# Kernel tuning notes

Measured on AMD Instinct MI355X. Metric: run time of the kernel, lower is better.

Reference implementation:

```python
import jax, jax.numpy as jnp
import numpy as np

N_NODES = 100000


def sage_conv(x, src, dst, w_self, w_nei, b):
    # mean aggregation over incoming edges (src -> dst)
    agg = jax.ops.segment_sum(x[src], dst, num_segments=N_NODES)          # [N, d]
    deg = jax.ops.segment_sum(jnp.ones((src.shape[0], 1), x.dtype), dst,
                              num_segments=N_NODES)                        # [N, 1]
    mean = agg / jnp.maximum(deg, 1.0)
    return x @ w_self + mean @ w_nei + b


def setup_inputs() -> dict:
    key = jax.random.key(0)
    ks = jax.random.split(key, 12)
    d_in, d_hid, d_out = 64, 64, 64
    E = 1600000
    s = lambda d: 1.0 / np.sqrt(d)
    return {
        "x": jax.random.normal(ks[0], (N_NODES, d_in), jnp.float32),
        "edge_index": jax.random.randint(ks[1], (2, E), 0, N_NODES, jnp.int64),
        "w_self1": jax.random.normal(ks[2], (d_in, d_hid), jnp.float32) * s(d_in),
        "w_nei1": jax.random.normal(ks[3], (d_in, d_hid), jnp.float32) * s(d_in),
        "b1": jnp.zeros((d_hid,), jnp.float32),
        "w_self2": jax.random.normal(ks[4], (d_hid, d_hid), jnp.float32) * s(d_hid),
        "w_nei2": jax.random.normal(ks[5], (d_hid, d_hid), jnp.float32) * s(d_hid),
        "b2": jnp.zeros((d_hid,), jnp.float32),
        "w_self3": jax.random.normal(ks[6], (d_hid, d_out), jnp.float32) * s(d_hid),
        "w_nei3": jax.random.normal(ks[7], (d_hid, d_out), jnp.float32) * s(d_hid),
        "b3": jnp.zeros((d_out,), jnp.float32),
    }


def reference(x, edge_index, w_self1, w_nei1, b1, w_self2, w_nei2, b2,
              w_self3, w_nei3, b3):
    src, dst = edge_index[0], edge_index[1]
    h = jax.nn.relu(sage_conv(x, src, dst, w_self1, w_nei1, b1))
    h = jax.nn.relu(sage_conv(h, src, dst, w_self2, w_nei2, b2))
    h = sage_conv(h, src, dst, w_self3, w_nei3, b3)
    return h
```

## Files before the change

### kernel.cpp

```cpp
#include <hip/hip_runtime.h>
#include <hip/hip_bf16.h>

#define PB   512
#define BN   64
#define CAP  1344

typedef short bf16x8 __attribute__((ext_vector_type(8)));
typedef float f32x4  __attribute__((ext_vector_type(4)));

__device__ __forceinline__ unsigned short f2bf(float f) {
    unsigned u = __float_as_uint(f);
    u += 0x7FFFu + ((u >> 16) & 1u);
    return (unsigned short)(u >> 16);
}

__global__ __launch_bounds__(256) void build_and_prep(
        const int* __restrict__ src, const int* __restrict__ dst,
        int* __restrict__ gcount, int* __restrict__ pairs, int E, int NB,
        const float* __restrict__ x, unsigned short* __restrict__ xb, int n8,
        const float* __restrict__ Ws1, const float* __restrict__ Wn1,
        const float* __restrict__ Ws2, const float* __restrict__ Wn2,
        const float* __restrict__ Ws3, const float* __restrict__ Wn3,
        unsigned short* __restrict__ bw) {
    const int tid = threadIdx.x;
    if (blockIdx.x < PB) {
        __shared__ int h[1664];
        for (int i = tid; i < NB; i += 256) h[i] = 0;
        __syncthreads();
        const int per = (E + PB - 1) / PB;
        const int s = blockIdx.x * per;
        const int e = min(E, s + per);
        for (int i = s + tid; i < e; i += 256) atomicAdd(&h[dst[i] >> 6], 1);
        __syncthreads();
        for (int b = tid; b < NB; b += 256) {
            const int c = h[b];
            h[b] = (c > 0) ? atomicAdd(&gcount[b], c) : 0;
        }
        __syncthreads();
        for (int i = s + tid; i < e; i += 256) {
            const int d = dst[i];
            const int b = d >> 6;
            const int slot = atomicAdd(&h[b], 1);
            if (slot < CAP)
                pairs[(size_t)b * CAP + slot] = src[i] | ((d & 63) << 20);
        }
    } else if (blockIdx.x < PB + 96) {
        const int i = (blockIdx.x - PB) * 256 + tid;
        const int w = i >> 13;
        const int r = i & 8191;
        const float* Ws = (w == 0) ? Ws1 : (w == 1) ? Ws2 : Ws3;
        const float* Wn = (w == 0) ? Wn1 : (w == 1) ? Wn2 : Wn3;
        const int j = r & 7;
        const int L = (r >> 3) & 63;
        const int t = (r >> 9) & 3;
        const int s = r >> 11;
        const int k = s * 32 + ((L >> 4) << 3) + j;
        const int n = t * 16 + (L & 15);
        const float v = (k < 64) ? Ws[k * 64 + n] : Wn[(k - 64) * 64 + n];
        bw[i] = f2bf(v);
    } else {
        const int g = (blockIdx.x - PB - 96) * 256 + tid;
        if (g >= n8) return;
        const float4 v0 = *(const float4*)(x + (size_t)g * 8);
        const float4 v1 = *(const float4*)(x + (size_t)g * 8 + 4);
        uint4 o;
        o.x = (unsigned)f2bf(v0.x) | ((unsigned)f2bf(v0.y) << 16);
        o.y = (unsigned)f2bf(v0.z) | ((unsigned)f2bf(v0.w) << 16);
        o.z = (unsigned)f2bf(v1.x) | ((unsigned)f2bf(v1.y) << 16);
        o.w = (unsigned)f2bf(v1.z) | ((unsigned)f2bf(v1.w) << 16);
        *(uint4*)(xb + (size_t)g * 8) = o;
    }
}

__global__ __launch_bounds__(256) void csr_finalize(const int* __restrict__ pairs,
                                                    const int* __restrict__ gcount,
                                                    int2* __restrict__ rowrange,
                                                    int* __restrict__ col, int N) {
    __shared__ int sp[CAP];
    __shared__ int h[64];
    __shared__ int tmp[64];
    __shared__ int cur[64];
    const int tid = threadIdx.x;
    const int b = blockIdx.x;
    const size_t base = (size_t)b * CAP;
    const int cnt = min(gcount[b], (int)CAP);

    for (int i = tid; i < cnt; i += 256) sp[i] = pairs[base + i];
    if (tid < 64) h[tid] = 0;
    __syncthreads();
    for (int i = tid; i < cnt; i += 256)
        atomicAdd(&h[(sp[i] >> 20) & 63], 1);
    __syncthreads();
    if (tid < 64) tmp[tid] = h[tid];
    __syncthreads();
    for (int off = 1; off < 64; off <<= 1) {
        int t = (tid >= off && tid < 64) ? tmp[tid - off] : 0;
        __syncthreads();
        if (tid < 64) tmp[tid] += t;
        __syncthreads();
    }
    if (tid < 64) {
        const int v = h[tid];
        const int excl = tmp[tid] - v;
        const int node = (b << 6) + tid;
        if (node < N) rowrange[node] = make_int2((int)base + excl, (int)base + excl + v);
        cur[tid] = excl;
    }
    __syncthreads();
    for (int i = tid; i < cnt; i += 256) {
        const int p = sp[i];
        const int slot = atomicAdd(&cur[(p >> 20) & 63], 1);
        col[base + slot] = p & 0xFFFFF;
    }
}

#define ACC8U(A, V)                                                   \
    A[0] += __uint_as_float((V).x << 16);                             \
    A[1] += __uint_as_float((V).x & 0xFFFF0000u);                     \
    A[2] += __uint_as_float((V).y << 16);                             \
    A[3] += __uint_as_float((V).y & 0xFFFF0000u);                     \
    A[4] += __uint_as_float((V).z << 16);                             \
    A[5] += __uint_as_float((V).z & 0xFFFF0000u);                     \
    A[6] += __uint_as_float((V).w << 16);                             \
    A[7] += __uint_as_float((V).w & 0xFFFF0000u);

__global__ __launch_bounds__(128) void sage_fused_kernel(
        const unsigned short* __restrict__ xin, const int* __restrict__ col,
        const int2* __restrict__ rowrange,
        const unsigned short* __restrict__ bswp, const float* __restrict__ bias,
        unsigned short* __restrict__ outb,
        float* __restrict__ outf,
        int N, int do_relu) {
    __shared__ __align__(16) unsigned short smean[32][72];

    const int tid = threadIdx.x;
    const int node0 = blockIdx.x * 32;
    const int lane = tid & 63;

    {
        const int nl = tid >> 2;
        const int node = node0 + nl;
        const int o = (tid & 3) * 8;
        float accA[8] = {0.f}, accB[8] = {0.f};
        float accC[8] = {0.f}, accD[8] = {0.f};
        float rd = 0.f;
        if (node < N) {
            const int2 rr = rowrange[node];
            const int beg = rr.x;
            const int end = rr.y;
            int i = beg;
            for (; i + 4 <= end; i += 4) {
                const int s0 = col[i + 0];
                const int s1 = col[i + 1];
                const int s2 = col[i + 2];
                const int s3 = col[i + 3];
                const unsigned short* p0 = xin + (size_t)s0 * 64 + o;
                const unsigned short* p1 = xin + (size_t)s1 * 64 + o;
                const unsigned short* p2 = xin + (size_t)s2 * 64 + o;
                const unsigned short* p3 = xin + (size_t)s3 * 64 + o;
                const uint4 a0 = *(const uint4*)(p0);
                const uint4 b0 = *(const uint4*)(p0 + 32);
                const uint4 a1 = *(const uint4*)(p1);
                const uint4 b1 = *(const uint4*)(p1 + 32);
                const uint4 a2 = *(const uint4*)(p2);
                const uint4 b2 = *(const uint4*)(p2 + 32);
                const uint4 a3 = *(const uint4*)(p3);
                const uint4 b3 = *(const uint4*)(p3 + 32);
                ACC8U(accA, a0) ACC8U(accB, b0)
                ACC8U(accC, a1) ACC8U(accD, b1)
                ACC8U(accA, a2) ACC8U(accB, b2)
                ACC8U(accC, a3) ACC8U(accD, b3)
            }
            for (; i < end; ++i) {
                const unsigned short* p = xin + (size_t)col[i] * 64 + o;
                const uint4 a = *(const uint4*)(p);
                const uint4 b = *(const uint4*)(p + 32);
                ACC8U(accA, a) ACC8U(accB, b)
            }
            rd = 1.0f / fmaxf((float)(end - beg), 1.0f);
        }
        uint4 o0, o1;
        {
            float m[8];
#pragma unroll
            for (int k = 0; k < 8; ++k) m[k] = (accA[k] + accC[k]) * rd;
            o0.x = (unsigned)f2bf(m[0]) | ((unsigned)f2bf(m[1]) << 16);
            o0.y = (unsigned)f2bf(m[2]) | ((unsigned)f2bf(m[3]) << 16);
            o0.z = (unsigned)f2bf(m[4]) | ((unsigned)f2bf(m[5]) << 16);
            o0.w = (unsigned)f2bf(m[6]) | ((unsigned)f2bf(m[7]) << 16);
#pragma unroll
            for (int k = 0; k < 8; ++k) m[k] = (accB[k] + accD[k]) * rd;
            o1.x = (unsigned)f2bf(m[0]) | ((unsigned)f2bf(m[1]) << 16);
            o1.y = (unsigned)f2bf(m[2]) | ((unsigned)f2bf(m[3]) << 16);
            o1.z = (unsigned)f2bf(m[4]) | ((unsigned)f2bf(m[5]) << 16);
            o1.w = (unsigned)f2bf(m[6]) | ((unsigned)f2bf(m[7]) << 16);
        }
        *(uint4*)(&smean[nl][o])      = o0;
        *(uint4*)(&smean[nl][o + 32]) = o1;
    }
    __syncthreads();

    const int wave = tid >> 6;
    const int m    = lane & 15;
    const int quad = lane >> 4;
    const int nw0  = node0 + wave * 16;

    int arow = nw0 + m;
    if (arow >= N) arow = N - 1;
    const unsigned short* xr = xin + (size_t)arow * 64 + quad * 8;

    f32x4 acc[4];
#pragma unroll
    for (int t = 0; t < 4; ++t) {
        const float b = bias[t * 16 + m];
        acc[t] = (f32x4){b, b, b, b};
    }

#pragma unroll
    for (int s = 0; s < 4; ++s) {
        bf16x8 a;
        if (s < 2) a = *(const bf16x8*)(xr + s * 32);
        else       a = *(const bf16x8*)(&smean[wave * 16 + m][(s - 2) * 32 + quad * 8]);
#pragma unroll
        for (int t = 0; t < 4; ++t) {
            const bf16x8 bf = *(const bf16x8*)(bswp + (((s * 4 + t) * 64 + lane) << 3));
            acc[t] = __builtin_amdgcn_mfma_f32_16x16x32_bf16(a, bf, acc[t], 0, 0, 0);
        }
    }

#pragma unroll
    for (int t = 0; t < 4; ++t) {
        const int colg = t * 16 + m;
#pragma unroll
        for (int r = 0; r < 4; ++r) {
            const int node = nw0 + quad * 4 + r;
            if (node < N) {
                float v = acc[t][r];
                if (do_relu) v = fmaxf(v, 0.f);
                if (outf) outf[(size_t)node * 64 + colg] = v;
                if (outb) outb[(size_t)node * 64 + colg] = f2bf(v);
            }
        }
    }
}

extern "C" void kernel_launch(void* const* d_in, const int* in_sizes, int n_in,
                              void* d_out, int out_size, void* d_ws, size_t ws_size,
                              hipStream_t stream) {
    const float* x   = (const float*)d_in[0];
    const int*   ei  = (const int*)d_in[1];
    const float* ws1 = (const float*)d_in[2];
    const float* wn1 = (const float*)d_in[3];
    const float* b1  = (const float*)d_in[4];
    const float* ws2 = (const float*)d_in[5];
    const float* wn2 = (const float*)d_in[6];
    const float* b2  = (const float*)d_in[7];
    const float* ws3 = (const float*)d_in[8];
    const float* wn3 = (const float*)d_in[9];
    const float* b3  = (const float*)d_in[10];

    const int N = in_sizes[0] / 64;
    const int E = in_sizes[1] / 2;
    const int* src = ei;
    const int* dst = ei + E;
    const int NB = (N + BN - 1) / BN;

    float* out = (float*)d_out;

    auto align256 = [](size_t v) { return (v + 255) / 256 * 256; };
    char* p = (char*)d_ws;
    int*  gcount   = (int*)p;  p += align256((size_t)NB * 4);
    int*  pairs    = (int*)p;  p += align256((size_t)NB * CAP * 4);
    int*  col      = (int*)p;  p += align256((size_t)NB * CAP * 4);
    int2* rowrange = (int2*)p; p += align256((size_t)N * 8);
    unsigned short* xb  = (unsigned short*)p; p += align256((size_t)N * 64 * 2);
    unsigned short* xb2 = (unsigned short*)p; p += align256((size_t)N * 64 * 2);
    unsigned short* bw  = (unsigned short*)p; p += align256(3 * 8192 * 2);

    const int n8 = N * 64 / 8;
    const int merged_blocks = PB + 96 + (n8 + 255) / 256;
    const int fused_blocks = (N + 31) / 32;

    hipMemsetAsync(gcount, 0, (size_t)NB * 4, stream);
    build_and_prep<<<merged_blocks, 256, 0, stream>>>(src, dst, gcount, pairs, E, NB,
                                                      x, xb, n8,
                                                      ws1, wn1, ws2, wn2, ws3, wn3, bw);
    csr_finalize<<<NB, 256, 0, stream>>>(pairs, gcount, rowrange, col, N);

    sage_fused_kernel<<<fused_blocks, 128, 0, stream>>>(xb,  col, rowrange, bw,         b1, xb2,     nullptr, N, 1);
    sage_fused_kernel<<<fused_blocks, 128, 0, stream>>>(xb2, col, rowrange, bw + 8192,  b2, xb,      nullptr, N, 1);
    sage_fused_kernel<<<fused_blocks, 128, 0, stream>>>(xb,  col, rowrange, bw + 16384, b3, nullptr, out,     N, 0);
}
```

Baseline: 258.4 us.

## Split bf16 features into low/high half planes and gather each half separately

Stores the bf16 node features as two separate 32-column planes (64 bytes per node each) and runs the neighbor gather in two passes, one per half, with an 8-wide unrolled inner loop. Each pass touches a smaller working set (6.4 MB per plane), which is meant to improve L2/MALL hit rates for the random gathers. The cost is reading the col indices twice per node and running a second gather loop, plus scattered 2-byte output stores split across two planes.

After: 286.4 us. 1.11x slower.

```diff
diff --git a/kernel.cpp b/kernel.cpp
--- a/kernel.cpp
+++ b/kernel.cpp
@@ -17,7 +17,8 @@
 __global__ __launch_bounds__(256) void build_and_prep(
         const int* __restrict__ src, const int* __restrict__ dst,
         int* __restrict__ gcount, int* __restrict__ pairs, int E, int NB,
-        const float* __restrict__ x, unsigned short* __restrict__ xb, int n8,
+        const float* __restrict__ x,
+        unsigned short* __restrict__ xlo, unsigned short* __restrict__ xhi, int n8,
         const float* __restrict__ Ws1, const float* __restrict__ Wn1,
         const float* __restrict__ Ws2, const float* __restrict__ Wn2,
         const float* __restrict__ Ws3, const float* __restrict__ Wn3,
@@ -68,7 +69,11 @@
         o.y = (unsigned)f2bf(v0.z) | ((unsigned)f2bf(v0.w) << 16);
         o.z = (unsigned)f2bf(v1.x) | ((unsigned)f2bf(v1.y) << 16);
         o.w = (unsigned)f2bf(v1.z) | ((unsigned)f2bf(v1.w) << 16);
-        *(uint4*)(xb + (size_t)g * 8) = o;
+        const int n = g >> 3;
+        const int c = (g & 7) * 8;
+        unsigned short* dstp = (c < 32) ? (xlo + (size_t)n * 32 + c)
+                                        : (xhi + (size_t)n * 32 + (c - 32));
+        *(uint4*)dstp = o;
     }
 }
 
@@ -125,10 +130,11 @@
     A[7] += __uint_as_float((V).w & 0xFFFF0000u);
 
 __global__ __launch_bounds__(128) void sage_fused_kernel(
-        const unsigned short* __restrict__ xin, const int* __restrict__ col,
-        const int2* __restrict__ rowrange,
+        const unsigned short* __restrict__ xlo, const unsigned short* __restrict__ xhi,
+        const int* __restrict__ col, const int2* __restrict__ rowrange,
         const unsigned short* __restrict__ bswp, const float* __restrict__ bias,
-        unsigned short* __restrict__ outb,
+        unsigned short* __restrict__ outlo,
+        unsigned short* __restrict__ outhi,
         float* __restrict__ outf,
         int N, int do_relu) {
     __shared__ __align__(16) unsigned short smean[32][72];
@@ -141,62 +147,59 @@
         const int nl = tid >> 2;
         const int node = node0 + nl;
         const int o = (tid & 3) * 8;
-        float accA[8] = {0.f}, accB[8] = {0.f};
-        float accC[8] = {0.f}, accD[8] = {0.f};
+        int beg = 0, end = 0;
         float rd = 0.f;
         if (node < N) {
             const int2 rr = rowrange[node];
-            const int beg = rr.x;
-            const int end = rr.y;
+            beg = rr.x;
+            end = rr.y;
+            rd = 1.0f / fmaxf((float)(end - beg), 1.0f);
+        }
+        const unsigned short* bases[2] = {xlo, xhi};
+#pragma unroll
+        for (int p = 0; p < 2; ++p) {
+            const unsigned short* B = bases[p];
+            float acc0[8] = {0.f}, acc1[8] = {0.f};
             int i = beg;
-            for (; i + 4 <= end; i += 4) {
-                const int s0 = col[i + 0];
-                const int s1 = col[i + 1];
-                const int s2 = col[i + 2];
-                const int s3 = col[i + 3];
-                const unsigned short* p0 = xin + (size_t)s0 * 64 + o;
-                const unsigned short* p1 = xin + (size_t)s1 * 64 + o;
-                const unsigned short* p2 = xin + (size_t)s2 * 64 + o;
-                const unsigned short* p3 = xin + (size_t)s3 * 64 + o;
-                const uint4 a0 = *(const uint4*)(p0);
-                const uint4 b0 = *(const uint4*)(p0 + 32);
-                const uint4 a1 = *(const uint4*)(p1);
-                const uint4 b1 = *(const uint4*)(p1 + 32);
-                const uint4 a2 = *(const uint4*)(p2);
-                const uint4 b2 = *(const uint4*)(p2 + 32);
-                const uint4 a3 = *(const uint4*)(p3);
-                const uint4 b3 = *(const uint4*)(p3 + 32);
-                ACC8U(accA, a0) ACC8U(accB, b0)
-                ACC8U(accC, a1) ACC8U(accD, b1)
-                ACC8U(accA, a2) ACC8U(accB, b2)
-                ACC8U(accC, a3) ACC8U(accD, b3)
+            for (; i + 8 <= end; i += 8) {
+                int s[8];
+#pragma unroll
+                for (int k = 0; k < 8; ++k) s[k] = col[i + k];
+                uint4 v[8];
+#pragma unroll
+                for (int k = 0; k < 8; ++k)
+                    v[k] = *(const uint4*)(B + (size_t)s[k] * 32 + o);
+#pragma unroll
+                for (int k = 0; k < 8; k += 2) {
+                    ACC8U(acc0, v[k]) ACC8U(acc1, v[k + 1])
+                }
+            }
+            if (i + 4 <= end) {
+                int s[4];
+#pragma unroll
+                for (int k = 0; k < 4; ++k) s[k] = col[i + k];
+                uint4 v[4];
+#pragma unroll
+                for (int k = 0; k < 4; ++k)
+                    v[k] = *(const uint4*)(B + (size_t)s[k] * 32 + o);
+                ACC8U(acc0, v[0]) ACC8U(acc1, v[1])
+                ACC8U(acc0, v[2]) ACC8U(acc1, v[3])
+                i += 4;
             }
             for (; i < end; ++i) {
-                const unsigned short* p = xin + (size_t)col[i] * 64 + o;
-                const uint4 a = *(const uint4*)(p);
-                const uint4 b = *(const uint4*)(p + 32);
-                ACC8U(accA, a) ACC8U(accB, b)
+                const uint4 v = *(const uint4*)(B + (size_t)col[i] * 32 + o);
+                ACC8U(acc0, v)
             }
-            rd = 1.0f / fmaxf((float)(end - beg), 1.0f);
-        }
-        uint4 o0, o1;
-        {
             float m[8];
 #pragma unroll
-            for (int k = 0; k < 8; ++k) m[k] = (accA[k] + accC[k]) * rd;
-            o0.x = (unsigned)f2bf(m[0]) | ((unsigned)f2bf(m[1]) << 16);
-            o0.y = (unsigned)f2bf(m[2]) | ((unsigned)f2bf(m[3]) << 16);
-            o0.z = (unsigned)f2bf(m[4]) | ((unsigned)f2bf(m[5]) << 16);
-            o0.w = (unsigned)f2bf(m[6]) | ((unsigned)f2bf(m[7]) << 16);
-#pragma unroll
-            for (int k = 0; k < 8; ++k) m[k] = (accB[k] + accD[k]) * rd;
-            o1.x = (unsigned)f2bf(m[0]) | ((unsigned)f2bf(m[1]) << 16);
-            o1.y = (unsigned)f2bf(m[2]) | ((unsigned)f2bf(m[3]) << 16);
-            o1.z = (unsigned)f2bf(m[4]) | ((unsigned)f2bf(m[5]) << 16);
-            o1.w = (unsigned)f2bf(m[6]) | ((unsigned)f2bf(m[7]) << 16);
-        }
-        *(uint4*)(&smean[nl][o])      = o0;
-        *(uint4*)(&smean[nl][o + 32]) = o1;
+            for (int k = 0; k < 8; ++k) m[k] = (acc0[k] + acc1[k]) * rd;
+            uint4 ov;
+            ov.x = (unsigned)f2bf(m[0]) | ((unsigned)f2bf(m[1]) << 16);
+            ov.y = (unsigned)f2bf(m[2]) | ((unsigned)f2bf(m[3]) << 16);
+            ov.z = (unsigned)f2bf(m[4]) | ((unsigned)f2bf(m[5]) << 16);
+            ov.w = (unsigned)f2bf(m[6]) | ((unsigned)f2bf(m[7]) << 16);
+            *(uint4*)(&smean[nl][p * 32 + o]) = ov;
+        }
     }
     __syncthreads();
 
@@ -207,7 +210,8 @@
 
     int arow = nw0 + m;
     if (arow >= N) arow = N - 1;
-    const unsigned short* xr = xin + (size_t)arow * 64 + quad * 8;
+    const unsigned short* xrl = xlo + (size_t)arow * 32 + quad * 8;
+    const unsigned short* xrh = xhi + (size_t)arow * 32 + quad * 8;
 
     f32x4 acc[4];
 #pragma unroll
@@ -219,8 +223,9 @@
 #pragma unroll
     for (int s = 0; s < 4; ++s) {
         bf16x8 a;
-        if (s < 2) a = *(const bf16x8*)(xr + s * 32);
-        else       a = *(const bf16x8*)(&smean[wave * 16 + m][(s - 2) * 32 + quad * 8]);
+        if (s == 0)      a = *(const bf16x8*)(xrl);
+        else if (s == 1) a = *(const bf16x8*)(xrh);
+        else             a = *(const bf16x8*)(&smean[wave * 16 + m][(s - 2) * 32 + quad * 8]);
 #pragma unroll
         for (int t = 0; t < 4; ++t) {
             const bf16x8 bf = *(const bf16x8*)(bswp + (((s * 4 + t) * 64 + lane) << 3));
@@ -238,7 +243,10 @@
                 float v = acc[t][r];
                 if (do_relu) v = fmaxf(v, 0.f);
                 if (outf) outf[(size_t)node * 64 + colg] = v;
-                if (outb) outb[(size_t)node * 64 + colg] = f2bf(v);
+                if (outlo) {
+                    if (colg < 32) outlo[(size_t)node * 32 + colg]        = f2bf(v);
+                    else           outhi[(size_t)node * 32 + (colg - 32)] = f2bf(v);
+                }
             }
         }
     }
@@ -273,9 +281,11 @@
     int*  pairs    = (int*)p;  p += align256((size_t)NB * CAP * 4);
     int*  col      = (int*)p;  p += align256((size_t)NB * CAP * 4);
     int2* rowrange = (int2*)p; p += align256((size_t)N * 8);
-    unsigned short* xb  = (unsigned short*)p; p += align256((size_t)N * 64 * 2);
-    unsigned short* xb2 = (unsigned short*)p; p += align256((size_t)N * 64 * 2);
-    unsigned short* bw  = (unsigned short*)p; p += align256(3 * 8192 * 2);
+    unsigned short* xlo  = (unsigned short*)p; p += align256((size_t)N * 32 * 2);
+    unsigned short* xhi  = (unsigned short*)p; p += align256((size_t)N * 32 * 2);
+    unsigned short* xlo2 = (unsigned short*)p; p += align256((size_t)N * 32 * 2);
+    unsigned short* xhi2 = (unsigned short*)p; p += align256((size_t)N * 32 * 2);
+    unsigned short* bw   = (unsigned short*)p; p += align256(3 * 8192 * 2);
 
     const int n8 = N * 64 / 8;
     const int merged_blocks = PB + 96 + (n8 + 255) / 256;
@@ -283,11 +293,11 @@
 
     hipMemsetAsync(gcount, 0, (size_t)NB * 4, stream);
     build_and_prep<<<merged_blocks, 256, 0, stream>>>(src, dst, gcount, pairs, E, NB,
-                                                      x, xb, n8,
+                                                      x, xlo, xhi, n8,
                                                       ws1, wn1, ws2, wn2, ws3, wn3, bw);
     csr_finalize<<<NB, 256, 0, stream>>>(pairs, gcount, rowrange, col, N);
 
-    sage_fused_kernel<<<fused_blocks, 128, 0, stream>>>(xb,  col, rowrange, bw,         b1, xb2,     nullptr, N, 1);
-    sage_fused_kernel<<<fused_blocks, 128, 0, stream>>>(xb2, col, rowrange, bw + 8192,  b2, xb,      nullptr, N, 1);
-    sage_fused_kernel<<<fused_blocks, 128, 0, stream>>>(xb,  col, rowrange, bw + 16384, b3, nullptr, out,     N, 0);
-}
+    sage_fused_kernel<<<fused_blocks, 128, 0, stream>>>(xlo,  xhi,  col, rowrange, bw,         b1, xlo2, xhi2, nullptr, N, 1);
+    sage_fused_kernel<<<fused_blocks, 128, 0, stream>>>(xlo2, xhi2, col, rowrange, bw + 8192,  b2, xlo,  xhi,  nullptr, N, 1);
+    sage_fused_kernel<<<fused_blocks, 128, 0, stream>>>(xlo,  xhi,  col, rowrange, bw + 16384, b3, nullptr, nullptr, out, N, 0);
+}
```

## Rewrite CSR finalize as single-wavefront kernel with shuffle scan and serial placement

Applied to the files above, without the earlier changes.

Replaces the 256-thread CSR finalize with a 64-thread single-wave kernel. The LDS scan with barriers becomes a wave shuffle scan, and the LDS atomic slot placement becomes a loop in which each lane scans all bucket entries and writes only its own node's edges. This removes barriers and shared atomics and makes the within-row order deterministic. In exchange each lane iterates over the whole bucket (~1000+ entries), giving serial work per block and scattered narrow writes, with only a quarter as many threads per block.

After: 325.4 us. 25.9% more time.

```diff
diff --git a/kernel.cpp b/kernel.cpp
--- a/kernel.cpp
+++ b/kernel.cpp
@@ -72,45 +72,42 @@
     }
 }
 
-__global__ __launch_bounds__(256) void csr_finalize(const int* __restrict__ pairs,
-                                                    const int* __restrict__ gcount,
-                                                    int2* __restrict__ rowrange,
-                                                    int* __restrict__ col, int N) {
+__global__ __launch_bounds__(64) void csr_wave_finalize(
+        const int* __restrict__ pairs, const int* __restrict__ gcount,
+        int2* __restrict__ rowrange, int* __restrict__ col, int N) {
     __shared__ int sp[CAP];
-    __shared__ int h[64];
-    __shared__ int tmp[64];
-    __shared__ int cur[64];
-    const int tid = threadIdx.x;
+    __shared__ int h[BN];
+    const int lane = threadIdx.x;
     const int b = blockIdx.x;
     const size_t base = (size_t)b * CAP;
     const int cnt = min(gcount[b], (int)CAP);
 
-    for (int i = tid; i < cnt; i += 256) sp[i] = pairs[base + i];
-    if (tid < 64) h[tid] = 0;
+    h[lane] = 0;
     __syncthreads();
-    for (int i = tid; i < cnt; i += 256)
-        atomicAdd(&h[(sp[i] >> 20) & 63], 1);
+    for (int i = lane; i < cnt; i += 64) {
+        const int p = pairs[base + i];
+        sp[i] = p;
+        atomicAdd(&h[(p >> 20) & 63], 1);
+    }
     __syncthreads();
-    if (tid < 64) tmp[tid] = h[tid];
-    __syncthreads();
+
+    const int deg = h[lane];
+    int pre = deg;
+#pragma unroll
     for (int off = 1; off < 64; off <<= 1) {
-        int t = (tid >= off && tid < 64) ? tmp[tid - off] : 0;
-        __syncthreads();
-        if (tid < 64) tmp[tid] += t;
-        __syncthreads();
-    }
-    if (tid < 64) {
-        const int v = h[tid];
-        const int excl = tmp[tid] - v;
-        const int node = (b << 6) + tid;
-        if (node < N) rowrange[node] = make_int2((int)base + excl, (int)base + excl + v);
-        cur[tid] = excl;
-    }
-    __syncthreads();
-    for (int i = tid; i < cnt; i += 256) {
+        const int t = __shfl_up(pre, off, 64);
+        if (lane >= off) pre += t;
+    }
+    const int excl = pre - deg;
+    const int node = (b << 6) + lane;
+    if (node < N)
+        rowrange[node] = make_int2((int)base + excl, (int)base + excl + deg);
+
+    int cur = (int)base + excl;
+    for (int i = 0; i < cnt; ++i) {
         const int p = sp[i];
-        const int slot = atomicAdd(&cur[(p >> 20) & 63], 1);
-        col[base + slot] = p & 0xFFFFF;
+        if (((p >> 20) & 63) == lane)
+            col[cur++] = p & 0xFFFFF;
     }
 }
 
@@ -285,7 +282,7 @@
     build_and_prep<<<merged_blocks, 256, 0, stream>>>(src, dst, gcount, pairs, E, NB,
                                                       x, xb, n8,
                                                       ws1, wn1, ws2, wn2, ws3, wn3, bw);
-    csr_finalize<<<NB, 256, 0, stream>>>(pairs, gcount, rowrange, col, N);
+    csr_wave_finalize<<<NB, 64, 0, stream>>>(pairs, gcount, rowrange, col, N);
 
     sage_fused_kernel<<<fused_blocks, 128, 0, stream>>>(xb,  col, rowrange, bw,         b1, xb2,     nullptr, N, 1);
     sage_fused_kernel<<<fused_blocks, 128, 0, stream>>>(xb2, col, rowrange, bw + 8192,  b2, xb,      nullptr, N, 1);
```
